# Performance work log

Hardware: AMD Instinct MI355X
Metric: run time of the kernel (lower is better)

## Reference

```python
import jax, jax.numpy as jnp
import numpy as np

N_BINS = 15
N = 1_000_000
C = 128


def setup_inputs() -> dict:
    key = jax.random.key(0)
    k1, k2 = jax.random.split(key)
    logits = jax.random.normal(k1, (N, C), dtype=jnp.float32)
    labels = jax.random.randint(k2, (N,), 0, C, dtype=jnp.int64)
    return {"logits": logits, "labels": labels}


def reference(logits, labels):
    # softmax -> per-sample confidence (max prob) and prediction (argmax)
    probs = jax.nn.softmax(logits, axis=1)
    confidences = jnp.max(probs, axis=1)          # [N]
    predictions = jnp.argmax(probs, axis=1)       # [N]
    accuracies = (predictions == labels).astype(jnp.float32)  # [N]

    # bin_lowers = linspace(0,1,n_bins+1)[:-1]; sample falls in bin i if
    # conf >= lower_i and conf < lower_{i+1} (last bin closed at 1.0).
    bin_lowers = jnp.linspace(0.0, 1.0, N_BINS + 1)[:-1]
    bin_idx = jnp.searchsorted(bin_lowers, confidences, side="right") - 1
    bin_idx = jnp.clip(bin_idx, 0, N_BINS - 1)

    correct = jax.ops.segment_sum(accuracies, bin_idx, num_segments=N_BINS)
    total = jax.ops.segment_sum(jnp.ones_like(accuracies), bin_idx, num_segments=N_BINS)
    # column 0: correct count in bin; column 1: incorrect count in bin
    bin_stats = jnp.stack([correct, total - correct], axis=1)  # [N_BINS, 2]
    return bin_stats
```

## Files before the change

### kernel.cpp

```cpp
#include <hip/hip_runtime.h>

#define N_BINS 15
#define NCLASS 128

typedef float fx4 __attribute__((ext_vector_type(4)));

__global__ void zero_out_kernel(float* __restrict__ out) {
    int i = threadIdx.x;
    if (i < 2 * N_BINS) out[i] = 0.0f;
}

__device__ __forceinline__ int dpp_xor1_i(int x) {
    return __builtin_amdgcn_mov_dpp(x, 0xB1, 0xF, 0xF, true);
}
__device__ __forceinline__ int dpp_xor2_i(int x) {
    return __builtin_amdgcn_mov_dpp(x, 0x4E, 0xF, 0xF, true);
}
__device__ __forceinline__ float dpp_xor1_f(float x) {
    return __int_as_float(dpp_xor1_i(__float_as_int(x)));
}
__device__ __forceinline__ float dpp_xor2_f(float x) {
    return __int_as_float(dpp_xor2_i(__float_as_int(x)));
}

__global__ __launch_bounds__(256, 4) void conf_hist_kernel(
        const float* __restrict__ logits,
        const int* __restrict__ labels,
        float* __restrict__ out,
        int n) {
    __shared__ int hist[2 * N_BINS];
    if (threadIdx.x < 2 * N_BINS) hist[threadIdx.x] = 0;
    __syncthreads();

    const int lane = threadIdx.x & 63;
    const int quad = lane >> 2;
    const int t = lane & 3;
    const int wavesPerBlock = blockDim.x >> 6;
    const int wave = blockIdx.x * wavesPerBlock + (threadIdx.x >> 6);
    const int numWaves = gridDim.x * wavesPerBlock;
    const int stride = numWaves * 16;

    int base = wave * 16;
    fx4 cA[8];
    int labA = 0;
    {
        const int s = base + quad;
        if (base < n && s < n) {
            const float* row = logits + (size_t)s * NCLASS + t * 4;
            #pragma unroll
            for (int j = 0; j < 8; ++j)
                cA[j] = __builtin_nontemporal_load((const fx4*)(row + j * 16));
            labA = labels[s];
        }
    }

    for (; base < n; base += stride) {
        const int s = base + quad;

        const int nbase = base + stride;
        const int ns = nbase + quad;
        fx4 cB[8];
        int labB = 0;
        if (nbase < n && ns < n) {
            const float* row = logits + (size_t)ns * NCLASS + t * 4;
            #pragma unroll
            for (int j = 0; j < 8; ++j)
                cB[j] = __builtin_nontemporal_load((const fx4*)(row + j * 16));
            labB = labels[ns];
        } else {
            #pragma unroll
            for (int j = 0; j < 8; ++j) cB[j] = (fx4)(0.0f);
        }

        if (s < n) {
            float m[8]; int mi[8];
            #pragma unroll
            for (int j = 0; j < 8; ++j) {
                float mm = cA[j][0]; int ii = 0;
                if (cA[j][1] > mm) { mm = cA[j][1]; ii = 1; }
                if (cA[j][2] > mm) { mm = cA[j][2]; ii = 2; }
                if (cA[j][3] > mm) { mm = cA[j][3]; ii = 3; }
                m[j] = mm; mi[j] = j * 16 + t * 4 + ii;
            }
            #pragma unroll
            for (int stp = 1; stp < 8; stp <<= 1) {
                #pragma unroll
                for (int j = 0; j < 8; j += 2 * stp) {
                    if (m[j + stp] > m[j]) { m[j] = m[j + stp]; mi[j] = mi[j + stp]; }
                }
            }
            float bm = m[0]; int bi = mi[0];

            {
                float om = dpp_xor1_f(bm); int oi = dpp_xor1_i(bi);
                if (om > bm || (om == bm && oi < bi)) { bm = om; bi = oi; }
            }
            {
                float om = dpp_xor2_f(bm); int oi = dpp_xor2_i(bi);
                if (om > bm || (om == bm && oi < bi)) { bm = om; bi = oi; }
            }

            float s4[8];
            #pragma unroll
            for (int j = 0; j < 8; ++j)
                s4[j] = (__expf(cA[j][0] - bm) + __expf(cA[j][1] - bm))
                      + (__expf(cA[j][2] - bm) + __expf(cA[j][3] - bm));
            float e = ((s4[0] + s4[1]) + (s4[2] + s4[3]))
                    + ((s4[4] + s4[5]) + (s4[6] + s4[7]));
            e += dpp_xor1_f(e);
            e += dpp_xor2_f(e);

            if (t == 0) {
                float conf = 1.0f / e;
                int bin = (int)(conf * (float)N_BINS);
                bin = bin > (N_BINS - 1) ? (N_BINS - 1) : (bin < 0 ? 0 : bin);
                int col = (bi == labA) ? 0 : 1;
                atomicAdd(&hist[bin * 2 + col], 1);
            }
        }

        #pragma unroll
        for (int j = 0; j < 8; ++j) cA[j] = cB[j];
        labA = labB;
    }

    __syncthreads();
    if (threadIdx.x < 2 * N_BINS) {
        int c = hist[threadIdx.x];
        if (c != 0) atomicAdd(&out[threadIdx.x], (float)c);
    }
}

extern "C" void kernel_launch(void* const* d_in, const int* in_sizes, int n_in,
                              void* d_out, int out_size, void* d_ws, size_t ws_size,
                              hipStream_t stream) {
    const float* logits = (const float*)d_in[0];
    const int*   labels = (const int*)d_in[1];
    float* out = (float*)d_out;
    const int n = in_sizes[1];

    zero_out_kernel<<<1, 64, 0, stream>>>(out);

    const int block = 256;
    const int grid = 2048;
    conf_hist_kernel<<<grid, block, 0, stream>>>(logits, labels, out, n);
}
```

Before: 629.2 us.

## Remap lanes to 8 per row and drop nontemporal loads

Each wave still handles 16 rows per iteration, but lanes are now split into octets of 8 that each cover one row, in two groups of 8 rows. Each lane loads four 16-byte chunks spaced 128 bytes apart instead of eight chunks spaced 64 bytes apart, so one load instruction covers more contiguous bytes per row. The cross-lane argmax and sum reductions gain a third step using ds_swizzle for xor-4. Nontemporal loads become plain loads, which changes cache behaviour for the streamed data.

Result: slower. 652.0 us (+3.6%).

```diff
diff --git a/kernel.cpp b/kernel.cpp
--- a/kernel.cpp
+++ b/kernel.cpp
@@ -16,11 +16,17 @@
 __device__ __forceinline__ int dpp_xor2_i(int x) {
     return __builtin_amdgcn_mov_dpp(x, 0x4E, 0xF, 0xF, true);
 }
+__device__ __forceinline__ int swz_xor4_i(int x) {
+    return __builtin_amdgcn_ds_swizzle(x, 0x101F);
+}
 __device__ __forceinline__ float dpp_xor1_f(float x) {
     return __int_as_float(dpp_xor1_i(__float_as_int(x)));
 }
 __device__ __forceinline__ float dpp_xor2_f(float x) {
     return __int_as_float(dpp_xor2_i(__float_as_int(x)));
+}
+__device__ __forceinline__ float swz_xor4_f(float x) {
+    return __int_as_float(swz_xor4_i(__float_as_int(x)));
 }
 
 __global__ __launch_bounds__(256, 4) void conf_hist_kernel(
@@ -33,95 +39,112 @@
     __syncthreads();
 
     const int lane = threadIdx.x & 63;
-    const int quad = lane >> 2;
-    const int t = lane & 3;
+    const int oct = lane >> 3;
+    const int q8 = lane & 7;
     const int wavesPerBlock = blockDim.x >> 6;
     const int wave = blockIdx.x * wavesPerBlock + (threadIdx.x >> 6);
     const int numWaves = gridDim.x * wavesPerBlock;
     const int stride = numWaves * 16;
 
+
     int base = wave * 16;
     fx4 cA[8];
-    int labA = 0;
+    int labAa = 0, labAb = 0;
     {
-        const int s = base + quad;
-        if (base < n && s < n) {
-            const float* row = logits + (size_t)s * NCLASS + t * 4;
+        const int sA = base + oct;
+        const int sB = base + 8 + oct;
+        if (sA < n) {
+            const float* rowA = logits + (size_t)sA * NCLASS + q8 * 4;
             #pragma unroll
-            for (int j = 0; j < 8; ++j)
-                cA[j] = __builtin_nontemporal_load((const fx4*)(row + j * 16));
-            labA = labels[s];
+            for (int j = 0; j < 4; ++j) cA[j] = *(const fx4*)(rowA + j * 32);
+            labAa = labels[sA];
+        }
+        if (sB < n) {
+            const float* rowB = logits + (size_t)sB * NCLASS + q8 * 4;
+            #pragma unroll
+            for (int j = 0; j < 4; ++j) cA[4 + j] = *(const fx4*)(rowB + j * 32);
+            labAb = labels[sB];
         }
     }
 
     for (; base < n; base += stride) {
-        const int s = base + quad;
-
         const int nbase = base + stride;
-        const int ns = nbase + quad;
         fx4 cB[8];
-        int labB = 0;
-        if (nbase < n && ns < n) {
-            const float* row = logits + (size_t)ns * NCLASS + t * 4;
-            #pragma unroll
-            for (int j = 0; j < 8; ++j)
-                cB[j] = __builtin_nontemporal_load((const fx4*)(row + j * 16));
-            labB = labels[ns];
-        } else {
-            #pragma unroll
-            for (int j = 0; j < 8; ++j) cB[j] = (fx4)(0.0f);
+        int labBa = 0, labBb = 0;
+        {
+            const int sA = nbase + oct;
+            const int sB = nbase + 8 + oct;
+            if (sA < n) {
+                const float* rowA = logits + (size_t)sA * NCLASS + q8 * 4;
+                #pragma unroll
+                for (int j = 0; j < 4; ++j) cB[j] = *(const fx4*)(rowA + j * 32);
+                labBa = labels[sA];
+            }
+            if (sB < n) {
+                const float* rowB = logits + (size_t)sB * NCLASS + q8 * 4;
+                #pragma unroll
+                for (int j = 0; j < 4; ++j) cB[4 + j] = *(const fx4*)(rowB + j * 32);
+                labBb = labels[sB];
+            }
         }
 
-        if (s < n) {
-            float m[8]; int mi[8];
-            #pragma unroll
-            for (int j = 0; j < 8; ++j) {
-                float mm = cA[j][0]; int ii = 0;
-                if (cA[j][1] > mm) { mm = cA[j][1]; ii = 1; }
-                if (cA[j][2] > mm) { mm = cA[j][2]; ii = 2; }
-                if (cA[j][3] > mm) { mm = cA[j][3]; ii = 3; }
-                m[j] = mm; mi[j] = j * 16 + t * 4 + ii;
-            }
-            #pragma unroll
-            for (int stp = 1; stp < 8; stp <<= 1) {
+        #pragma unroll
+        for (int g = 0; g < 2; ++g) {
+            const int s = base + g * 8 + oct;
+            if (s < n) {
+                const fx4* c = &cA[g * 4];
+                const int lab = g ? labAb : labAa;
+
+                float m[4]; int mi[4];
                 #pragma unroll
-                for (int j = 0; j < 8; j += 2 * stp) {
-                    if (m[j + stp] > m[j]) { m[j] = m[j + stp]; mi[j] = mi[j + stp]; }
+                for (int j = 0; j < 4; ++j) {
+                    float mm = c[j][0]; int ii = 0;
+                    if (c[j][1] > mm) { mm = c[j][1]; ii = 1; }
+                    if (c[j][2] > mm) { mm = c[j][2]; ii = 2; }
+                    if (c[j][3] > mm) { mm = c[j][3]; ii = 3; }
+                    m[j] = mm; mi[j] = j * 32 + q8 * 4 + ii;
                 }
-            }
-            float bm = m[0]; int bi = mi[0];
+                if (m[1] > m[0]) { m[0] = m[1]; mi[0] = mi[1]; }
+                if (m[3] > m[2]) { m[2] = m[3]; mi[2] = mi[3]; }
+                if (m[2] > m[0]) { m[0] = m[2]; mi[0] = mi[2]; }
+                float bm = m[0]; int bi = mi[0];
 
-            {
-                float om = dpp_xor1_f(bm); int oi = dpp_xor1_i(bi);
-                if (om > bm || (om == bm && oi < bi)) { bm = om; bi = oi; }
-            }
-            {
-                float om = dpp_xor2_f(bm); int oi = dpp_xor2_i(bi);
-                if (om > bm || (om == bm && oi < bi)) { bm = om; bi = oi; }
-            }
+                {
+                    float om = dpp_xor1_f(bm); int oi = dpp_xor1_i(bi);
+                    if (om > bm || (om == bm && oi < bi)) { bm = om; bi = oi; }
+                }
+                {
+                    float om = dpp_xor2_f(bm); int oi = dpp_xor2_i(bi);
+                    if (om > bm || (om == bm && oi < bi)) { bm = om; bi = oi; }
+                }
+                {
+                    float om = swz_xor4_f(bm); int oi = swz_xor4_i(bi);
+                    if (om > bm || (om == bm && oi < bi)) { bm = om; bi = oi; }
+                }
 
-            float s4[8];
-            #pragma unroll
-            for (int j = 0; j < 8; ++j)
-                s4[j] = (__expf(cA[j][0] - bm) + __expf(cA[j][1] - bm))
-                      + (__expf(cA[j][2] - bm) + __expf(cA[j][3] - bm));
-            float e = ((s4[0] + s4[1]) + (s4[2] + s4[3]))
-                    + ((s4[4] + s4[5]) + (s4[6] + s4[7]));
-            e += dpp_xor1_f(e);
-            e += dpp_xor2_f(e);
+                float s4[4];
+                #pragma unroll
+                for (int j = 0; j < 4; ++j)
+                    s4[j] = (__expf(c[j][0] - bm) + __expf(c[j][1] - bm))
+                          + (__expf(c[j][2] - bm) + __expf(c[j][3] - bm));
+                float e = (s4[0] + s4[1]) + (s4[2] + s4[3]);
+                e += dpp_xor1_f(e);
+                e += dpp_xor2_f(e);
+                e += swz_xor4_f(e);
 
-            if (t == 0) {
-                float conf = 1.0f / e;
-                int bin = (int)(conf * (float)N_BINS);
-                bin = bin > (N_BINS - 1) ? (N_BINS - 1) : (bin < 0 ? 0 : bin);
-                int col = (bi == labA) ? 0 : 1;
-                atomicAdd(&hist[bin * 2 + col], 1);
+                if (q8 == 0) {
+                    float conf = 1.0f / e;
+                    int bin = (int)(conf * (float)N_BINS);
+                    bin = bin > (N_BINS - 1) ? (N_BINS - 1) : (bin < 0 ? 0 : bin);
+                    int col = (bi == lab) ? 0 : 1;
+                    atomicAdd(&hist[bin * 2 + col], 1);
+                }
             }
         }
 
         #pragma unroll
         for (int j = 0; j < 8; ++j) cA[j] = cB[j];
-        labA = labB;
+        labAa = labBa; labAb = labBb;
     }
 
     __syncthreads();
```
